# Kernel optimization log

Hardware: AMD Instinct MI355X
Metric: run time of the kernel (lower is better)

Reference implementation:

```python
import jax, jax.numpy as jnp
import numpy as np

# static config (matches init_kwargs)
B, H, W, C = 8, 64, 64, 512
HEADS, WS, SHIFT = 16, 8, 4
N = WS * WS
HIDDEN = 4 * C
HEAD_DIM = C // HEADS
SCALE = HEAD_DIM ** -0.5
EPS = 1e-3  # keras LayerNormalization default epsilon


def _rel_pos_index(ws):
    # replicates tf.meshgrid default 'xy' indexing used in the source
    coords = np.stack(np.meshgrid(np.arange(ws), np.arange(ws)))  # [2, ws, ws]
    cf = coords.reshape(2, -1)
    rel = (cf[:, :, None] - cf[:, None, :]).transpose(1, 2, 0)  # [N, N, 2]
    rel[:, :, 0] += ws - 1
    rel[:, :, 1] += ws - 1
    rel[:, :, 0] *= 2 * ws - 1
    return jnp.asarray(rel.sum(-1))  # [N, N] int


def _attn_mask(h, w, ws, shift):
    img = np.zeros((h, w), dtype=np.float32)
    cnt = 0
    for hs in (slice(0, -ws), slice(-ws, -shift), slice(-shift, None)):
        for wsl in (slice(0, -ws), slice(-ws, -shift), slice(-shift, None)):
            img[hs, wsl] = cnt
            cnt += 1
    mw = img.reshape(h // ws, ws, w // ws, ws).transpose(0, 2, 1, 3).reshape(-1, ws * ws)  # [nW, N]
    diff = mw[:, None, :] - mw[:, :, None]
    return jnp.asarray(np.where(diff != 0, -100.0, 0.0).astype(np.float32))  # [nW, N, N]


REL_IDX = _rel_pos_index(WS)
ATTN_MASK = _attn_mask(H, W, WS, SHIFT)
NW = (H // WS) * (W // WS)


def _ln(x, g, b):
    mu = jnp.mean(x, -1, keepdims=True)
    var = jnp.mean(jnp.square(x - mu), -1, keepdims=True)
    return (x - mu) * jax.lax.rsqrt(var + EPS) * g + b


def setup_inputs() -> dict:
    key = jax.random.key(0)
    ks = jax.random.split(key, 14)
    s = 0.02
    return {
        "x": jax.random.normal(ks[0], (B, H * W, C), jnp.float32),
        "norm1_g": jnp.ones((C,), jnp.float32),
        "norm1_b": jnp.zeros((C,), jnp.float32),
        "qkv_w": jax.random.normal(ks[1], (C, 3 * C), jnp.float32) * s,
        "qkv_b": jnp.zeros((3 * C,), jnp.float32),
        "rpb_table": jax.random.normal(ks[2], ((2 * WS - 1) ** 2, HEADS), jnp.float32) * s,
        "proj_w": jax.random.normal(ks[3], (C, C), jnp.float32) * s,
        "proj_b": jnp.zeros((C,), jnp.float32),
        "norm2_g": jnp.ones((C,), jnp.float32),
        "norm2_b": jnp.zeros((C,), jnp.float32),
        "fc1_w": jax.random.normal(ks[4], (C, HIDDEN), jnp.float32) * s,
        "fc1_b": jnp.zeros((HIDDEN,), jnp.float32),
        "fc2_w": jax.random.normal(ks[5], (HIDDEN, C), jnp.float32) * s,
        "fc2_b": jnp.zeros((C,), jnp.float32),
    }


def reference(x, norm1_g, norm1_b, qkv_w, qkv_b, rpb_table, proj_w, proj_b,
              norm2_g, norm2_b, fc1_w, fc1_b, fc2_w, fc2_b):
    shortcut = x
    h = _ln(x, norm1_g, norm1_b).reshape(B, H, W, C)
    # cyclic shift (SW-MSA)
    h = jnp.roll(h, (-SHIFT, -SHIFT), axis=(1, 2))
    # window partition -> (B*nW, N, C)
    h = h.reshape(B, H // WS, WS, W // WS, WS, C).transpose(0, 1, 3, 2, 4, 5)
    h = h.reshape(B * NW, N, C)
    # qkv
    qkv = (h @ qkv_w + qkv_b).reshape(B * NW, N, 3, HEADS, HEAD_DIM).transpose(2, 0, 3, 1, 4)
    q, k, v = qkv[0] * SCALE, qkv[1], qkv[2]  # each [Bw, heads, N, hd]
    attn = jnp.einsum('bhnd,bhmd->bhnm', q, k)  # [Bw, heads, N, N]
    bias = rpb_table[REL_IDX.reshape(-1)].reshape(N, N, HEADS).transpose(2, 0, 1)
    attn = attn + bias[None]
    # shifted-window mask, per source: mask add -> softmax -> softmax AGAIN (source quirk)
    attn = attn.reshape(B, NW, HEADS, N, N) + ATTN_MASK[None, :, None]
    attn = attn.reshape(B * NW, HEADS, N, N)
    attn = jax.nn.softmax(attn, axis=-1)
    attn = jax.nn.softmax(attn, axis=-1)
    o = jnp.einsum('bhnm,bhmd->bhnd', attn, v).transpose(0, 2, 1, 3).reshape(B * NW, N, C)
    o = o @ proj_w + proj_b
    # window reverse + reverse shift
    o = o.reshape(B, H // WS, W // WS, WS, WS, C).transpose(0, 1, 3, 2, 4, 5).reshape(B, H, W, C)
    o = jnp.roll(o, (SHIFT, SHIFT), axis=(1, 2)).reshape(B, H * W, C)
    x = shortcut + o
    # MLP: source applies gelu twice (Dense activation + explicit gelu)
    y = _ln(x, norm2_g, norm2_b)
    y = jax.nn.gelu(jax.nn.gelu(y @ fc1_w + fc1_b, approximate=False), approximate=False)
    y = y @ fc2_w + fc2_b
    return x + y
```

## Files before the change

### kernel.cpp

```cpp
#include <hip/hip_runtime.h>
#include <hip/hip_bf16.h>
#include <math.h>


typedef unsigned short ushort_t;
typedef __attribute__((ext_vector_type(8))) short short8;
typedef __attribute__((ext_vector_type(8))) __bf16 bf16x8;
typedef __attribute__((ext_vector_type(4))) float f32x4;

#define DEVINL __device__ __forceinline__

union frag_u { short8 s; bf16x8 b; };

DEVINL float bf2f(ushort_t u){ union {unsigned int i; float f;} c; c.i = ((unsigned)u)<<16; return c.f; }
DEVINL ushort_t f2bf(float f){ union {unsigned int i; float f;} c; c.f = f; unsigned r = c.i + 0x7fffu + ((c.i>>16)&1u); return (ushort_t)(r>>16); }

typedef const __attribute__((address_space(1))) void* gas_t;
typedef __attribute__((address_space(3))) void* las_t;
DEVINL void load_lds16(const void* g, void* l) {
  __builtin_amdgcn_global_load_lds((gas_t)g, (las_t)l, 16, 0, 0);
}

DEVINL float gelu_fast(float v){
  float z  = fabsf(v) * 0.70710678118654752f;
  float t  = __builtin_amdgcn_rcpf(fmaf(0.47047f, z, 1.0f));
  float p  = t * fmaf(t, fmaf(t, 0.7478556f, -0.0958798f), 0.3480242f);
  float e  = __expf(-z*z);
  float er = fmaf(-p, e, 1.0f);
  float hs = (v >= 0.f) ? 0.5f : -0.5f;
  return v * fmaf(hs, er, 0.5f);
}

DEVINL int win_map_row(int t){
  int bw = t >> 6, n = t & 63;
  int b  = bw >> 6, wdx = bw & 63;
  int wh = wdx >> 3, ww = wdx & 7;
  int r  = n >> 3,  c  = n & 7;
  int hh = (wh*8 + r + 4) & 63;
  int w2 = (ww*8 + c + 4) & 63;
  return (b << 12) + (hh << 6) + w2;
}

__global__ void transpose_all(const float* __restrict__ qkv_w, const float* __restrict__ proj_w,
                              const float* __restrict__ fc1_w, const float* __restrict__ fc2_w,
                              ushort_t* __restrict__ wqT, ushort_t* __restrict__ wpT,
                              ushort_t* __restrict__ w1T, ushort_t* __restrict__ w2T){
  __shared__ float t[32][33];
  int bid = blockIdx.x;
  const float* in; ushort_t* out; int R, Ccols, bx, by;
  if (bid < 768)      { in=qkv_w;  out=wqT; R=512;  Ccols=1536; bx=(bid%48)*32;        by=(bid/48)*32; }
  else if (bid < 1024){ int b=bid-768;  in=proj_w; out=wpT; R=512;  Ccols=512;  bx=(b%16)*32; by=(b/16)*32; }
  else if (bid < 2048){ int b=bid-1024; in=fc1_w;  out=w1T; R=512;  Ccols=2048; bx=(b%64)*32; by=(b/64)*32; }
  else                { int b=bid-2048; in=fc2_w;  out=w2T; R=2048; Ccols=512;  bx=(b%16)*32; by=(b/16)*32; }
  int x = threadIdx.x, y = threadIdx.y;
  #pragma unroll
  for (int i=0;i<32;i+=8) t[y+i][x] = in[(size_t)(by+y+i)*Ccols + bx + x];
  __syncthreads();
  #pragma unroll
  for (int i=0;i<32;i+=8) out[(size_t)(bx+y+i)*R + by + x] = f2bf(t[x][y+i]);
}

__global__ __launch_bounds__(256) void ln_kernel(const float* __restrict__ in,
    const float* __restrict__ g, const float* __restrict__ bta,
    ushort_t* __restrict__ out, int windowed){
  int tid = threadIdx.x; int l = tid & 63; int w = tid >> 6;
  int t = blockIdx.x * 4 + w;
  int src = windowed ? win_map_row(t) : t;
  const float* row = in + (size_t)src * 512;
  float4 v0 = *(const float4*)(row + l*8);
  float4 v1 = *(const float4*)(row + l*8 + 4);
  float f[8] = {v0.x,v0.y,v0.z,v0.w, v1.x,v1.y,v1.z,v1.w};
  float s=0.f, s2=0.f;
  #pragma unroll
  for (int j=0;j<8;j++){ s += f[j]; s2 += f[j]*f[j]; }
  #pragma unroll
  for (int m=1;m<64;m<<=1){ s += __shfl_xor(s,m); s2 += __shfl_xor(s2,m); }
  float mu  = s * (1.f/512.f);
  float var = s2*(1.f/512.f) - mu*mu;
  float rs  = rsqrtf(var + 1e-3f);
  float4 g0 = *(const float4*)(g + l*8),   g1 = *(const float4*)(g + l*8 + 4);
  float4 b0 = *(const float4*)(bta + l*8), b1 = *(const float4*)(bta + l*8 + 4);
  float gg[8] = {g0.x,g0.y,g0.z,g0.w, g1.x,g1.y,g1.z,g1.w};
  float bb[8] = {b0.x,b0.y,b0.z,b0.w, b1.x,b1.y,b1.z,b1.w};
  short8 o;
  #pragma unroll
  for (int j=0;j<8;j++) o[j] = (short)f2bf((f[j]-mu)*rs*gg[j] + bb[j]);
  *(short8*)(out + (size_t)t*512 + l*8) = o;
}

template<int EPI>
__global__ __launch_bounds__(256, 2) void gemm_bt(
    const ushort_t* __restrict__ A, const ushort_t* __restrict__ Bt,
    const float* __restrict__ bias, void* __restrict__ Cout_v,
    const float* __restrict__ xres, int M, int N, int K)
{
  __shared__ ushort_t lAB[2*128*32];
  ushort_t* lA = lAB;
  ushort_t* lB = lAB + 128*32;
  int tid = threadIdx.x; int l = tid & 63; int w = tid >> 6;
  int m0 = blockIdx.x*128, n0 = blockIdx.y*128;
  int wr = (w>>1)*64, wc = (w&1)*64;
  int lr = l & 15, lk = l >> 4;

  f32x4 acc[4][4] = {};
  for (int k0 = 0; k0 < K; k0 += 32) {
    #pragma unroll
    for (int i=0;i<2;i++){
      int s   = i*256 + tid;
      int row = s >> 2;
      int cg  = ((s&3) - (row>>1)) & 3;
      ushort_t* ldst  = lA + (size_t)(i*256 + w*64)*8;
      load_lds16(A  + (size_t)(m0+row)*K + (k0 + cg*8), ldst);
      ushort_t* ldstB = lB + (size_t)(i*256 + w*64)*8;
      load_lds16(Bt + (size_t)(n0+row)*K + (k0 + cg*8), ldstB);
    }
    __syncthreads();
    bf16x8 af[4], bfr[4];
    #pragma unroll
    for (int m=0;m<4;m++){
      int row  = wr + m*16 + lr;
      int slot = row*4 + ((lk + (row>>1)) & 3);
      af[m] = *(const bf16x8*)(lA + slot*8);
    }
    #pragma unroll
    for (int n=0;n<4;n++){
      int row  = wc + n*16 + lr;
      int slot = row*4 + ((lk + (row>>1)) & 3);
      bfr[n] = *(const bf16x8*)(lB + slot*8);
    }
    #pragma unroll
    for (int m=0;m<4;m++)
      #pragma unroll
      for (int n=0;n<4;n++)
        acc[m][n] = __builtin_amdgcn_mfma_f32_16x16x32_bf16(af[m], bfr[n], acc[m][n], 0,0,0);
    __syncthreads();
  }

  if (EPI == 0 || EPI == 1){
    ushort_t* tw = lAB + w*1152;
    int row = l >> 2, cc = l & 3;
    #pragma unroll
    for (int m=0;m<4;m++){
      #pragma unroll
      for (int n=0;n<4;n++){
        float bz = bias[n0 + wc + n*16 + lr];
        #pragma unroll
        for (int r=0;r<4;r++){
          float v = acc[m][n][r] + bz;
          if (EPI == 1) v = gelu_fast(gelu_fast(v));
          tw[(lk*4+r)*72 + n*16 + lr] = f2bf(v);
        }
      }
      short8 p0 = *(const short8*)(tw + row*72 + cc*16);
      short8 p1 = *(const short8*)(tw + row*72 + cc*16 + 8);
      int grow = m0 + wr + m*16 + row;
      int col  = n0 + wc + cc*16;
      *(short8*)&((ushort_t*)Cout_v)[(size_t)grow*N + col]     = p0;
      *(short8*)&((ushort_t*)Cout_v)[(size_t)grow*N + col + 8] = p1;
    }
  } else {
    #pragma unroll
    for (int m=0;m<4;m++){
      int rloc = wr + m*16 + lk*4;
      #pragma unroll
      for (int n=0;n<4;n++){
        int col = n0 + wc + n*16 + lr;
        float bz = bias[col];
        #pragma unroll
        for (int r=0;r<4;r++){
          int grow = m0 + rloc + r;
          float v = acc[m][n][r] + bz;
          if (EPI == 2){
            int row2 = win_map_row(grow);
            size_t off = (size_t)row2*512 + col;
            ((float*)Cout_v)[off] = xres[off] + v;
          } else {
            size_t off = (size_t)grow*N + col;
            ((float*)Cout_v)[off] += v;
          }
        }
      }
    }
  }
}

#define G_STAGE(G, base, h, tt, LB) do { \
    load_lds16((G) + (base) + (size_t)((h)*128)*K    + (size_t)(tt)*64, &lds[(LB) + (h)*8192 +        w*512]); \
    load_lds16((G) + (base) + (size_t)((h)*128+64)*K + (size_t)(tt)*64, &lds[(LB) + (h)*8192 + 4096 + w*512]); \
  } while(0)

#define NOWAIT
#define VM4 asm volatile("s_waitcnt vmcnt(4)" ::: "memory")

#define PHASE(mp, STAGE_STMT, EXTRA) do { \
    bf16x8 a0 = *(const bf16x8*)&lds[ALb + aoff[2*(mp)  ][0]]; \
    bf16x8 a1 = *(const bf16x8*)&lds[ALb + aoff[2*(mp)  ][1]]; \
    bf16x8 a2 = *(const bf16x8*)&lds[ALb + aoff[2*(mp)+1][0]]; \
    bf16x8 a3 = *(const bf16x8*)&lds[ALb + aoff[2*(mp)+1][1]]; \
    STAGE_STMT; \
    EXTRA; \
    __builtin_amdgcn_s_barrier(); \
    asm volatile("s_waitcnt lgkmcnt(0)" ::: "memory"); \
    __builtin_amdgcn_sched_barrier(0); \
    __builtin_amdgcn_s_setprio(1); \
    _Pragma("unroll") \
    for (int nf=0; nf<4; nf++){ \
      acc[2*(mp)  ][nf] = __builtin_amdgcn_mfma_f32_16x16x32_bf16(a0, bfr[nf][0], acc[2*(mp)  ][nf], 0,0,0); \
      acc[2*(mp)  ][nf] = __builtin_amdgcn_mfma_f32_16x16x32_bf16(a1, bfr[nf][1], acc[2*(mp)  ][nf], 0,0,0); \
      acc[2*(mp)+1][nf] = __builtin_amdgcn_mfma_f32_16x16x32_bf16(a2, bfr[nf][0], acc[2*(mp)+1][nf], 0,0,0); \
      acc[2*(mp)+1][nf] = __builtin_amdgcn_mfma_f32_16x16x32_bf16(a3, bfr[nf][1], acc[2*(mp)+1][nf], 0,0,0); \
    } \
    __builtin_amdgcn_s_setprio(0); \
    __builtin_amdgcn_sched_barrier(0); \
    __builtin_amdgcn_s_barrier(); \
  } while(0)

template<int EPI>
__global__ __launch_bounds__(512, 2) void gemm256(
    const ushort_t* __restrict__ A, const ushort_t* __restrict__ Bt,
    const float* __restrict__ bias, void* __restrict__ Cout_v,
    const float* __restrict__ xres, int M, int N, int K)
{
  __shared__ ushort_t lds[65536];
  const int tid = threadIdx.x; const int l = tid & 63; const int w = tid >> 6;
  const int wm = w >> 2, wn = w & 3;
  const int m0 = blockIdx.x*256, n0 = blockIdx.y*256;
  const int lr = l & 15, lk = l >> 4;
  const int nt = K >> 6;

  const int r0 = tid >> 3;
  const int kc = ((tid & 7) - r0) & 7;
  const size_t aRow0 = (size_t)(m0 + r0) * K + kc * 8;
  const size_t bRow0 = (size_t)(n0 + r0) * K + kc * 8;

  int aoff[8][2], boff[4][2];
  #pragma unroll
  for (int mf=0; mf<8; mf++){
    int row = wm*128 + mf*16 + lr;
    #pragma unroll
    for (int kh=0; kh<2; kh++){ int c = kh*4 + lk; aoff[mf][kh] = (row*8 + ((c + row)&7))*8; }
  }
  #pragma unroll
  for (int nf=0; nf<4; nf++){
    int row = wn*64 + nf*16 + lr;
    #pragma unroll
    for (int kh=0; kh<2; kh++){ int c = kh*4 + lk; boff[nf][kh] = (row*8 + ((c + row)&7))*8; }
  }

  f32x4 acc[8][4] = {};

  G_STAGE(A,  aRow0, 0, 0, 0);
  G_STAGE(A,  aRow0, 1, 0, 0);
  G_STAGE(Bt, bRow0, 0, 0, 16384);
  G_STAGE(Bt, bRow0, 1, 0, 16384);
  G_STAGE(Bt, bRow0, 0, 1, 32768+16384);
  G_STAGE(Bt, bRow0, 1, 1, 32768+16384);
  VM4;
  __builtin_amdgcn_s_barrier();

  for (int t = 0; t < nt; ++t) {
    const int b   = t & 1;
    const int ALb = b*32768, BLb = ALb + 16384;
    const int ALn = (b^1)*32768;
    const int t1  = (t+1 < nt) ? t+1 : t;
    const int t2  = (t+2 < nt) ? t+2 : t;

    bf16x8 bfr[4][2];
    #pragma unroll
    for (int nf=0; nf<4; nf++){
      bfr[nf][0] = *(const bf16x8*)&lds[BLb + boff[nf][0]];
      bfr[nf][1] = *(const bf16x8*)&lds[BLb + boff[nf][1]];
    }
    PHASE(0, G_STAGE(A,  aRow0, 0, t1, ALn), NOWAIT);
    PHASE(1, G_STAGE(A,  aRow0, 1, t1, ALn), NOWAIT);
    PHASE(2, G_STAGE(Bt, bRow0, 0, t2, BLb), NOWAIT);
    PHASE(3, G_STAGE(Bt, bRow0, 1, t2, BLb), VM4);
  }

  asm volatile("s_waitcnt vmcnt(0)" ::: "memory");
  __builtin_amdgcn_s_barrier();

  int erow = l >> 2, ecc = l & 3;
  if (EPI == 0){
    ushort_t* tw = lds + w*1152;
    #pragma unroll
    for (int mf=0; mf<8; mf++){
      #pragma unroll
      for (int nf=0; nf<4; nf++){
        float bz = bias[n0 + wn*64 + nf*16 + lr];
        #pragma unroll
        for (int rg=0; rg<4; rg++)
          tw[(lk*4+rg)*72 + nf*16 + lr] = f2bf(acc[mf][nf][rg] + bz);
      }
      short8 p0 = *(const short8*)(tw + erow*72 + ecc*16);
      short8 p1 = *(const short8*)(tw + erow*72 + ecc*16 + 8);
      int grow = m0 + wm*128 + mf*16 + erow;
      int col  = n0 + wn*64 + ecc*16;
      *(short8*)&((ushort_t*)Cout_v)[(size_t)grow*N + col]     = p0;
      *(short8*)&((ushort_t*)Cout_v)[(size_t)grow*N + col + 8] = p1;
    }
  } else {
    float* twf = (float*)lds + w*1152;
    #pragma unroll
    for (int mf=0; mf<8; mf++){
      #pragma unroll
      for (int nf=0; nf<4; nf++){
        float bz = bias[n0 + wn*64 + nf*16 + lr];
        #pragma unroll
        for (int rg=0; rg<4; rg++)
          twf[(lk*4+rg)*72 + nf*16 + lr] = acc[mf][nf][rg] + bz;
      }
      int grow = m0 + wm*128 + mf*16 + erow;
      int col  = n0 + wn*64 + ecc*16;
      float4 q0 = *(const float4*)(twf + erow*72 + ecc*16);
      float4 q1 = *(const float4*)(twf + erow*72 + ecc*16 + 4);
      float4 q2 = *(const float4*)(twf + erow*72 + ecc*16 + 8);
      float4 q3 = *(const float4*)(twf + erow*72 + ecc*16 + 12);
      size_t off;
      if (EPI == 2){
        int row2 = win_map_row(grow);
        off = (size_t)row2*512 + col;
        float4 x0 = *(const float4*)(xres + off);
        float4 x1 = *(const float4*)(xres + off + 4);
        float4 x2 = *(const float4*)(xres + off + 8);
        float4 x3 = *(const float4*)(xres + off + 12);
        q0 = make_float4(q0.x+x0.x, q0.y+x0.y, q0.z+x0.z, q0.w+x0.w);
        q1 = make_float4(q1.x+x1.x, q1.y+x1.y, q1.z+x1.z, q1.w+x1.w);
        q2 = make_float4(q2.x+x2.x, q2.y+x2.y, q2.z+x2.z, q2.w+x2.w);
        q3 = make_float4(q3.x+x3.x, q3.y+x3.y, q3.z+x3.z, q3.w+x3.w);
      } else {
        off = (size_t)grow*N + col;
        float* o = (float*)Cout_v;
        float4 x0 = *(const float4*)(o + off);
        float4 x1 = *(const float4*)(o + off + 4);
        float4 x2 = *(const float4*)(o + off + 8);
        float4 x3 = *(const float4*)(o + off + 12);
        q0 = make_float4(q0.x+x0.x, q0.y+x0.y, q0.z+x0.z, q0.w+x0.w);
        q1 = make_float4(q1.x+x1.x, q1.y+x1.y, q1.z+x1.z, q1.w+x1.w);
        q2 = make_float4(q2.x+x2.x, q2.y+x2.y, q2.z+x2.z, q2.w+x2.w);
        q3 = make_float4(q3.x+x3.x, q3.y+x3.y, q3.z+x3.z, q3.w+x3.w);
      }
      float* o = (float*)Cout_v;
      *(float4*)(o + off)      = q0;
      *(float4*)(o + off + 4)  = q1;
      *(float4*)(o + off + 8)  = q2;
      *(float4*)(o + off + 12) = q3;
    }
  }
}

DEVINL int band3(int t){ return (t<56) ? 0 : ((t<60) ? 1 : 2); }

__global__ __launch_bounds__(256) void attn_kernel(const ushort_t* __restrict__ qkv,
    const float* __restrict__ rpb, ushort_t* __restrict__ o)
{
  __shared__ ushort_t sP[4][64*64];
  __shared__ ushort_t sV[4][64*32];
  int tid = threadIdx.x; int l = tid & 63; int w = tid >> 6;
  int p = blockIdx.x*4 + w;
  int bw = p >> 4, head = p & 15;
  int lr = l & 15, lk = l >> 4;
  const ushort_t* base = qkv + (size_t)bw*64*1536 + head*32;

  #pragma unroll
  for (int c=0;c<4;c++){
    int idx = c*64 + l;
    int row = idx >> 2, cc = idx & 3;
    load_lds16(base + 1024 + (size_t)row*1536 + cc*8, &sV[w][0] + c*512);
  }

  bf16x8 qf[4], kf[4];
  #pragma unroll
  for (int m=0;m<4;m++) qf[m] = *(const bf16x8*)(base +       (size_t)(m*16+lr)*1536 + lk*8);
  #pragma unroll
  for (int m=0;m<4;m++) kf[m] = *(const bf16x8*)(base + 512 + (size_t)(m*16+lr)*1536 + lk*8);

  f32x4 s[4][4] = {};
  #pragma unroll
  for (int m=0;m<4;m++)
    #pragma unroll
    for (int n=0;n<4;n++)
      s[m][n] = __builtin_amdgcn_mfma_f32_16x16x32_bf16(qf[m], kf[n], s[m][n], 0,0,0);

  int wdx = bw & 63; int wh = wdx >> 3, ww = wdx & 7;
  const float SCALE = 0.17677669529663687f;
  #pragma unroll
  for (int m=0;m<4;m++){
    #pragma unroll
    for (int r=0;r<4;r++){
      int i  = m*16 + lk*4 + r;
      int ri = band3(wh*8 + (i>>3))*3 + band3(ww*8 + (i&7));
      int ix = i & 7, iy = i >> 3;
      #pragma unroll
      for (int n=0;n<4;n++){
        int j   = n*16 + lr;
        int rj  = band3(wh*8 + (j>>3))*3 + band3(ww*8 + (j&7));
        int idx = 15*(ix - (j&7) + 7) + (iy - (j>>3) + 7);
        float bv = rpb[idx*16 + head];
        float mk = (ri == rj) ? 0.f : -100.f;
        s[m][n][r] = s[m][n][r]*SCALE + bv + mk;
      }
    }
  }

  #pragma unroll
  for (int pass=0; pass<2; pass++){
    #pragma unroll
    for (int m=0;m<4;m++){
      #pragma unroll
      for (int r=0;r<4;r++){
        float mx = fmaxf(fmaxf(s[m][0][r], s[m][1][r]), fmaxf(s[m][2][r], s[m][3][r]));
        #pragma unroll
        for (int d=1;d<16;d<<=1) mx = fmaxf(mx, __shfl_xor(mx, d));
        float sum = 0.f;
        #pragma unroll
        for (int n=0;n<4;n++){ float e = __expf(s[m][n][r]-mx); s[m][n][r]=e; sum += e; }
        #pragma unroll
        for (int d=1;d<16;d<<=1) sum += __shfl_xor(sum, d);
        float inv = 1.f/sum;
        #pragma unroll
        for (int n=0;n<4;n++) s[m][n][r] = s[m][n][r]*inv;
      }
    }
  }

  ushort_t* pl = &sP[w][0];
  #pragma unroll
  for (int m=0;m<4;m++)
    #pragma unroll
    for (int r=0;r<4;r++){
      int i = m*16 + lk*4 + r;
      #pragma unroll
      for (int n=0;n<4;n++){
        int j = n*16 + lr;
        int byte = i*128 + ((j*2) ^ ((i&7)<<4));
        pl[byte>>1] = f2bf(s[m][n][r]);
      }
    }

  asm volatile("s_waitcnt vmcnt(0)" ::: "memory");
  const ushort_t* vl = &sV[w][0];
  frag_u vf[2][2];
  #pragma unroll
  for (int kb=0;kb<2;kb++)
    #pragma unroll
    for (int nb=0;nb<2;nb++){
      #pragma unroll
      for (int j=0;j<8;j++){
        int k = kb*32 + lk*8 + j;
        vf[kb][nb].s[j] = (short)vl[k*32 + nb*16 + lr];
      }
    }

  f32x4 oacc[4][2] = {};
  #pragma unroll
  for (int m=0;m<4;m++){
    #pragma unroll
    for (int kb=0;kb<2;kb++){
      int row  = m*16 + lr;
      int byte = row*128 + ((kb*64 + lk*16) ^ ((row&7)<<4));
      bf16x8 pf = *(const bf16x8*)(pl + (byte>>1));
      #pragma unroll
      for (int nb=0;nb<2;nb++)
        oacc[m][nb] = __builtin_amdgcn_mfma_f32_16x16x32_bf16(pf, vf[kb][nb].b, oacc[m][nb], 0,0,0);
    }
  }

  ushort_t* orow = o + (size_t)bw*64*512 + head*32;
  #pragma unroll
  for (int m=0;m<4;m++)
    #pragma unroll
    for (int nb=0;nb<2;nb++)
      #pragma unroll
      for (int r=0;r<4;r++){
        int i = m*16 + lk*4 + r;
        int d = nb*16 + lr;
        orow[(size_t)i*512 + d] = f2bf(oacc[m][nb][r]);
      }
}

extern "C" void kernel_launch(void* const* d_in, const int* in_sizes, int n_in,
                              void* d_out, int out_size, void* d_ws, size_t ws_size,
                              hipStream_t stream) {
  const float* x      = (const float*)d_in[0];
  const float* n1g    = (const float*)d_in[1];
  const float* n1b    = (const float*)d_in[2];
  const float* qkv_w  = (const float*)d_in[3];
  const float* qkv_b  = (const float*)d_in[4];
  const float* rpb    = (const float*)d_in[5];
  const float* proj_w = (const float*)d_in[6];
  const float* proj_b = (const float*)d_in[7];
  const float* n2g    = (const float*)d_in[8];
  const float* n2b    = (const float*)d_in[9];
  const float* fc1_w  = (const float*)d_in[10];
  const float* fc1_b  = (const float*)d_in[11];
  const float* fc2_w  = (const float*)d_in[12];
  const float* fc2_b  = (const float*)d_in[13];
  float* out = (float*)d_out;

  ushort_t* ws = (ushort_t*)d_ws;
  size_t off = 0;
  ushort_t* wqT = ws + off; off += (size_t)1536*512;
  ushort_t* wpT = ws + off; off += (size_t)512*512;
  ushort_t* w1T = ws + off; off += (size_t)2048*512;
  ushort_t* w2T = ws + off; off += (size_t)512*2048;
  ushort_t* R1  = ws + off; off += (size_t)32768*512;
  ushort_t* R2  = ws + off; off += (size_t)32768*2048;
  if (ws_size < off*sizeof(ushort_t)) return;

  transpose_all<<<3072, dim3(32,8), 0, stream>>>(qkv_w, proj_w, fc1_w, fc2_w, wqT, wpT, w1T, w2T);

  ln_kernel<<<8192, 256, 0, stream>>>(x, n1g, n1b, R1, 1);
  gemm256<0><<<dim3(128, 6), 512, 0, stream>>>(R1, wqT, qkv_b, R2, nullptr, 32768, 1536, 512);
  attn_kernel<<<2048, 256, 0, stream>>>(R2, rpb, R1);
  gemm256<2><<<dim3(128, 2), 512, 0, stream>>>(R1, wpT, proj_b, out, x, 32768, 512, 512);
  ln_kernel<<<8192, 256, 0, stream>>>(out, n2g, n2b, R1, 0);
  gemm_bt<1><<<dim3(256, 16), 256, 0, stream>>>(R1, w1T, fc1_b, R2, nullptr, 32768, 2048, 512);
  gemm256<3><<<dim3(128, 2), 512, 0, stream>>>(R2, w2T, fc2_b, out, nullptr, 32768, 512, 2048);
}
```

Before: 423.7 us.

## Remap GEMM tiles across XCDs and replace double-GELU with LDS lookup table

Switches all GEMM launches to a 1D grid and remaps block IDs so that consecutive logical tiles land on the same XCD chiplet (assuming round-robin dispatch across 8 XCDs), improving L2 locality for shared A/B panels. The fc1 epilogue replaces the two nested erf-based GELU evaluations with a 1024-entry linear-interpolation table over [-4,4], built in LDS per block, with clamps to identity or zero outside that range. This cuts transcendental work in the epilogue but adds per-block table construction, extra LDS use that may affect occupancy, and approximation error in the activation.

```diff
diff --git a/kernel.cpp b/kernel.cpp
--- a/kernel.cpp
+++ b/kernel.cpp
@@ -39,6 +39,13 @@
   int hh = (wh*8 + r + 4) & 63;
   int w2 = (ww*8 + c + 4) & 63;
   return (b << 12) + (hh << 6) + w2;
+}
+
+DEVINL void remap_mn(int bid, int nwg, int nbn, int BM, int BN, int& m0, int& n0){
+  int q    = nwg >> 3;
+  int lbid = (bid & 7)*q + (bid >> 3);
+  m0 = (lbid / nbn) * BM;
+  n0 = (lbid % nbn) * BN;
 }
 
 __global__ void transpose_all(const float* __restrict__ qkv_w, const float* __restrict__ proj_w,
@@ -92,15 +99,28 @@
 __global__ __launch_bounds__(256, 2) void gemm_bt(
     const ushort_t* __restrict__ A, const ushort_t* __restrict__ Bt,
     const float* __restrict__ bias, void* __restrict__ Cout_v,
-    const float* __restrict__ xres, int M, int N, int K)
+    const float* __restrict__ xres, int M, int N, int K, int nbn)
 {
   __shared__ ushort_t lAB[2*128*32];
+  __shared__ float2 g2tab[1024];
   ushort_t* lA = lAB;
   ushort_t* lB = lAB + 128*32;
   int tid = threadIdx.x; int l = tid & 63; int w = tid >> 6;
-  int m0 = blockIdx.x*128, n0 = blockIdx.y*128;
+  int m0, n0;
+  remap_mn(blockIdx.x, gridDim.x, nbn, 128, 128, m0, n0);
   int wr = (w>>1)*64, wc = (w&1)*64;
   int lr = l & 15, lk = l >> 4;
+
+  if (EPI == 1){
+    #pragma unroll
+    for (int i=0;i<4;i++){
+      int idx = tid*4 + i;
+      float vi = -4.f + (float)idx*(1.f/128.f);
+      float a  = gelu_fast(gelu_fast(vi));
+      float b  = gelu_fast(gelu_fast(vi + (1.f/128.f)));
+      g2tab[idx] = make_float2(a, b - a);
+    }
+  }
 
   f32x4 acc[4][4] = {};
   for (int k0 = 0; k0 < K; k0 += 32) {
@@ -147,7 +167,15 @@
         #pragma unroll
         for (int r=0;r<4;r++){
           float v = acc[m][n][r] + bz;
-          if (EPI == 1) v = gelu_fast(gelu_fast(v));
+          if (EPI == 1){
+            float u  = fminf(fmaxf((v + 4.f)*128.f, 0.f), 1023.999f);
+            int   iu = (int)u;
+            float fr = u - (float)iu;
+            float2 pq = g2tab[iu];
+            float rr = fmaf(fr, pq.y, pq.x);
+            rr = (v >  4.f) ? v   : rr;
+            v  = (v < -4.f) ? 0.f : rr;
+          }
           tw[(lk*4+r)*72 + n*16 + lr] = f2bf(v);
         }
       }
@@ -219,12 +247,13 @@
 __global__ __launch_bounds__(512, 2) void gemm256(
     const ushort_t* __restrict__ A, const ushort_t* __restrict__ Bt,
     const float* __restrict__ bias, void* __restrict__ Cout_v,
-    const float* __restrict__ xres, int M, int N, int K)
+    const float* __restrict__ xres, int M, int N, int K, int nbn)
 {
   __shared__ ushort_t lds[65536];
   const int tid = threadIdx.x; const int l = tid & 63; const int w = tid >> 6;
   const int wm = w >> 2, wn = w & 3;
-  const int m0 = blockIdx.x*256, n0 = blockIdx.y*256;
+  int m0, n0;
+  remap_mn(blockIdx.x, gridDim.x, nbn, 256, 256, m0, n0);
   const int lr = l & 15, lk = l >> 4;
   const int nt = K >> 6;
 
@@ -511,10 +540,10 @@
   transpose_all<<<3072, dim3(32,8), 0, stream>>>(qkv_w, proj_w, fc1_w, fc2_w, wqT, wpT, w1T, w2T);
 
   ln_kernel<<<8192, 256, 0, stream>>>(x, n1g, n1b, R1, 1);
-  gemm256<0><<<dim3(128, 6), 512, 0, stream>>>(R1, wqT, qkv_b, R2, nullptr, 32768, 1536, 512);
+  gemm256<0><<<768, 512, 0, stream>>>(R1, wqT, qkv_b, R2, nullptr, 32768, 1536, 512, 6);
   attn_kernel<<<2048, 256, 0, stream>>>(R2, rpb, R1);
-  gemm256<2><<<dim3(128, 2), 512, 0, stream>>>(R1, wpT, proj_b, out, x, 32768, 512, 512);
+  gemm256<2><<<256, 512, 0, stream>>>(R1, wpT, proj_b, out, x, 32768, 512, 512, 2);
   ln_kernel<<<8192, 256, 0, stream>>>(out, n2g, n2b, R1, 0);
-  gemm_bt<1><<<dim3(256, 16), 256, 0, stream>>>(R1, w1T, fc1_b, R2, nullptr, 32768, 2048, 512);
-  gemm256<3><<<dim3(128, 2), 512, 0, stream>>>(R2, w2T, fc2_b, out, nullptr, 32768, 512, 2048);
-}
+  gemm_bt<1><<<4096, 256, 0, stream>>>(R1, w1T, fc1_b, R2, nullptr, 32768, 2048, 512, 16);
+  gemm256<3><<<256, 512, 0, stream>>>(R2, w2T, fc2_b, out, nullptr, 32768, 512, 2048, 2);
+}
```

Result: faster. 393.7 us (-7.1%).
